# Kernel tuning notes

Measured on AMD Instinct MI355X. Metric: run time of the kernel, lower is better.

## Reference

```python
import jax, jax.numpy as jnp
import numpy as np

B, S, E = 2, 2048, 2048
H, KV, HD = 16, 4, 128          # attn heads, kv heads, head_dim = E//H
GROUPS = H // KV
I = 8192                        # intermediate_size
EPS = 1e-6
ROPE_THETA = 10000.0
SCALE = HD ** -0.5


def _rope_tables(seq_len, head_dim, dtype=jnp.float32):
    inv_freq = 1.0 / (ROPE_THETA ** (jnp.arange(0, head_dim, 2, dtype=jnp.float32) / head_dim))
    pos = jnp.arange(seq_len, dtype=jnp.float32)
    ang = pos[:, None] * inv_freq[None, :]            # [S, HD/2]
    emb = jnp.concatenate([ang, ang], axis=-1)        # [S, HD]
    return jnp.cos(emb).astype(dtype), jnp.sin(emb).astype(dtype)


def _rotate_half(x):
    x1, x2 = jnp.split(x, 2, axis=-1)
    return jnp.concatenate([-x2, x1], axis=-1)


def _apply_rope(x, cos, sin):
    # x: [B, h, S, HD]; cos/sin: [S, HD]
    return x * cos[None, None] + _rotate_half(x) * sin[None, None]


def _rmsnorm(x, w, eps=EPS):
    var = jnp.mean(jnp.square(x), axis=-1, keepdims=True)
    return x * jax.lax.rsqrt(var + eps) * w


def setup_inputs() -> dict:
    key = jax.random.key(0)
    ks = jax.random.split(key, 12)
    sd = lambda fan_in: 1.0 / np.sqrt(fan_in)
    inp = {
        "x": jax.random.normal(ks[0], (B, S, E), dtype=jnp.float32),
        "attn_mask": jnp.zeros((B, 1, S, S), dtype=jnp.bool_),
        "wq": jax.random.normal(ks[1], (E, E), dtype=jnp.float32) * sd(E),
        "bq": jnp.zeros((E,), dtype=jnp.float32),
        "wkv": jax.random.normal(ks[2], (2 * KV * HD, E), dtype=jnp.float32) * sd(E),
        "bkv": jnp.zeros((2 * KV * HD,), dtype=jnp.float32),
        "wo": jax.random.normal(ks[3], (E, E), dtype=jnp.float32) * sd(E),
        "w_gate": jax.random.normal(ks[4], (I, E), dtype=jnp.float32) * sd(E),
        "w_up": jax.random.normal(ks[5], (I, E), dtype=jnp.float32) * sd(E),
        "w_down": jax.random.normal(ks[6], (E, I), dtype=jnp.float32) * sd(I),
        "norm1_w": jnp.ones((E,), dtype=jnp.float32),
        "norm2_w": jnp.ones((E,), dtype=jnp.float32),
    }
    return inp


def reference(x, attn_mask, wq, bq, wkv, bkv, wo, w_gate, w_up, w_down, norm1_w, norm2_w):
    # ---- attention block ----
    y = _rmsnorm(x, norm1_w)
    q = y @ wq.T + bq                                     # [B,S,E]
    kv = y @ wkv.T + bkv                                  # [B,S,2*KV*HD]
    k, v = jnp.split(kv, 2, axis=-1)
    q = q.reshape(B, S, H, HD).transpose(0, 2, 1, 3)      # [B,H,S,HD]
    k = k.reshape(B, S, KV, HD).transpose(0, 2, 1, 3)     # [B,KV,S,HD]
    v = v.reshape(B, S, KV, HD).transpose(0, 2, 1, 3)
    cos, sin = _rope_tables(S, HD, dtype=q.dtype)
    q = _apply_rope(q, cos, sin)
    k = _apply_rope(k, cos, sin)
    # GQA expand kv heads
    k = jnp.repeat(k, GROUPS, axis=1)                     # [B,H,S,HD]
    v = jnp.repeat(v, GROUPS, axis=1)
    # NOTE: source Qwen2Attention.forward never applies attn_mask — faithful here.
    scores = jnp.einsum('bhsd,bhtd->bhst', q, k) * SCALE  # [B,H,S,S]
    attn = jax.nn.softmax(scores, axis=-1)
    o = jnp.einsum('bhst,bhtd->bhsd', attn, v)            # [B,H,S,HD]
    o = o.transpose(0, 2, 1, 3).reshape(B, S, E) @ wo.T
    x = x + o
    # ---- MLP block (SwiGLU) ----
    y = _rmsnorm(x, norm2_w)
    h = jax.nn.silu(y @ w_gate.T) * (y @ w_up.T)          # [B,S,I]
    x = x + h @ w_down.T
    return x
```

## Files before the change

kernel.cpp:

```cpp
#include <hip/hip_runtime.h>

typedef __bf16 bf16;
typedef __bf16 bf16x8 __attribute__((ext_vector_type(8)));
typedef __bf16 bf16x4 __attribute__((ext_vector_type(4)));
typedef float f32x4 __attribute__((ext_vector_type(4)));

#define DEV __device__ __forceinline__

constexpr int B_ = 2, S_ = 2048, E_ = 2048, H_ = 16, KVH_ = 4, HD_ = 128, I_ = 8192;
constexpr int KVROW = 2 * KVH_ * HD_;
constexpr float EPS_ = 1e-6f;
constexpr float SCALE_ = 0.08838834764831845f;

DEV void gload_lds16(const bf16* g, bf16* l) {
  __builtin_amdgcn_global_load_lds(
      (const __attribute__((address_space(1))) void*)g,
      (__attribute__((address_space(3))) void*)l, 16, 0, 0);
}

__global__ __launch_bounds__(256) void cvt_k(const float* __restrict__ src,
                                             bf16* __restrict__ dst, int n) {
  for (int i = (blockIdx.x * 256 + threadIdx.x) * 8; i < n; i += gridDim.x * 256 * 8) {
    const float4* p = (const float4*)(src + i);
    float4 a = p[0], b = p[1];
    bf16x8 o;
    o[0] = (bf16)a.x; o[1] = (bf16)a.y; o[2] = (bf16)a.z; o[3] = (bf16)a.w;
    o[4] = (bf16)b.x; o[5] = (bf16)b.y; o[6] = (bf16)b.z; o[7] = (bf16)b.w;
    *(bf16x8*)(dst + i) = o;
  }
}

template <typename InT>
__global__ __launch_bounds__(256) void rmsnorm_k(const InT* __restrict__ x,
                                                 const float* __restrict__ w,
                                                 bf16* __restrict__ y) {
  const int row = blockIdx.x, t = threadIdx.x;
  const size_t base = (size_t)row * E_ + t * 8;
  float v[8];
  if constexpr (sizeof(InT) == 2) {
    bf16x8 d = *(const bf16x8*)(x + base);
#pragma unroll
    for (int j = 0; j < 8; ++j) v[j] = (float)d[j];
  } else {
    const float4* p = (const float4*)(x + base);
    float4 a = p[0], b2 = p[1];
    v[0]=a.x; v[1]=a.y; v[2]=a.z; v[3]=a.w; v[4]=b2.x; v[5]=b2.y; v[6]=b2.z; v[7]=b2.w;
  }
  float ss = 0.f;
#pragma unroll
  for (int j = 0; j < 8; ++j) ss += v[j] * v[j];
#pragma unroll
  for (int off = 32; off; off >>= 1) ss += __shfl_xor(ss, off);
  __shared__ float red[4];
  if ((t & 63) == 0) red[t >> 6] = ss;
  __syncthreads();
  ss = red[0] + red[1] + red[2] + red[3];
  const float sc = rsqrtf(ss * (1.0f / E_) + EPS_);
  const float4* wp = (const float4*)(w + t * 8);
  float4 wa = wp[0], wb = wp[1];
  float wv[8] = {wa.x, wa.y, wa.z, wa.w, wb.x, wb.y, wb.z, wb.w};
  bf16x8 o;
#pragma unroll
  for (int j = 0; j < 8; ++j) o[j] = (bf16)(v[j] * sc * wv[j]);
  *(bf16x8*)(y + base) = o;
}

__global__ __launch_bounds__(256) void rope_k(bf16* __restrict__ q, bf16* __restrict__ kvb) {
  const int gid = blockIdx.x * 256 + threadIdx.x;
  const int d = gid & 63;
  const int r = gid >> 6;
  const int hh = r % (H_ + KVH_);
  const int s = (r / (H_ + KVH_)) % S_;
  const int b = r / ((H_ + KVH_) * S_);
  bf16* p = (hh < H_) ? (q + (size_t)(b * S_ + s) * E_ + hh * HD_)
                      : (kvb + (size_t)(b * S_ + s) * KVROW + (hh - H_) * HD_);
  const float invf = exp2f(-(float)d * (13.287712379549449f / 64.f));
  float sn, cs;
  sincosf((float)s * invf, &sn, &cs);
  const float x1 = (float)p[d], x2 = (float)p[d + 64];
  p[d] = (bf16)(x1 * cs - x2 * sn);
  p[d + 64] = (bf16)(x2 * cs + x1 * sn);
}

template <int EPI, bool WB>
__global__ __launch_bounds__(256, 2) void gemm_bt(const bf16* __restrict__ A,
                                                  const void* __restrict__ Wp,
                                                  const float* __restrict__ bias,
                                                  const void* __restrict__ ext,
                                                  void* __restrict__ out,
                                                  int M, int N, int K) {
  constexpr int BK = 64;
  __shared__ bf16 As[128 * BK];
  __shared__ bf16 Bs[128 * BK];
  const int t = threadIdx.x, lane = t & 63, w = t >> 6;
  const int g = lane >> 4, l15 = lane & 15;
  const int bm = blockIdx.y, bn = blockIdx.x;
  const int wm = w >> 1, wn = w & 1;
  f32x4 acc[4][4];
#pragma unroll
  for (int i = 0; i < 4; ++i)
#pragma unroll
    for (int j = 0; j < 4; ++j) acc[i][j] = {0.f, 0.f, 0.f, 0.f};

  const bf16* Ab = A + (size_t)bm * 128 * K;

  for (int k0 = 0; k0 < K; k0 += BK) {
    __syncthreads();
#pragma unroll
    for (int i = 0; i < 4; ++i) {
      const int c = t + i * 256;
      const int row = c >> 3, slot = c & 7;
      gload_lds16(Ab + (size_t)row * K + k0 + ((slot ^ (row & 7)) << 3), &As[c * 8]);
    }
    if constexpr (WB) {
      const bf16* Wb = (const bf16*)Wp + (size_t)bn * 128 * K;
#pragma unroll
      for (int i = 0; i < 4; ++i) {
        const int c = t + i * 256;
        const int row = c >> 3, slot = c & 7;
        gload_lds16(Wb + (size_t)row * K + k0 + ((slot ^ (row & 7)) << 3), &Bs[c * 8]);
      }
    } else {
      const float* Wb = (const float*)Wp + (size_t)bn * 128 * K;
#pragma unroll
      for (int i = 0; i < 4; ++i) {
        const int c = t + i * 256;
        const int row = c >> 3, slot = c & 7;
        const float4* wp = (const float4*)(Wb + (size_t)row * K + k0 + slot * 8);
        float4 w0 = wp[0], w1 = wp[1];
        bf16x8 pk;
        pk[0] = (bf16)w0.x; pk[1] = (bf16)w0.y; pk[2] = (bf16)w0.z; pk[3] = (bf16)w0.w;
        pk[4] = (bf16)w1.x; pk[5] = (bf16)w1.y; pk[6] = (bf16)w1.z; pk[7] = (bf16)w1.w;
        *(bf16x8*)&Bs[row * BK + ((slot ^ (row & 7)) << 3)] = pk;
      }
    }
    __syncthreads();
#pragma unroll
    for (int ks = 0; ks < 2; ++ks) {
      bf16x8 af[4], bfv[4];
#pragma unroll
      for (int mt = 0; mt < 4; ++mt) {
        const int row = wm * 64 + mt * 16 + l15;
        af[mt] = *(const bf16x8*)&As[row * BK + (((ks * 4 + g) ^ (row & 7)) << 3)];
      }
#pragma unroll
      for (int nt = 0; nt < 4; ++nt) {
        const int row = wn * 64 + nt * 16 + l15;
        bfv[nt] = *(const bf16x8*)&Bs[row * BK + (((ks * 4 + g) ^ (row & 7)) << 3)];
      }
#pragma unroll
      for (int mt = 0; mt < 4; ++mt)
#pragma unroll
        for (int nt = 0; nt < 4; ++nt)
          acc[mt][nt] = __builtin_amdgcn_mfma_f32_16x16x32_bf16(af[mt], bfv[nt], acc[mt][nt], 0, 0, 0);
    }
  }

  const int row0 = bm * 128 + wm * 64;
  const int col0 = bn * 128 + wn * 64;
#pragma unroll
  for (int nt = 0; nt < 4; ++nt) {
    const int col = col0 + nt * 16 + l15;
    const float bv = bias ? bias[col] : 0.f;
#pragma unroll
    for (int mt = 0; mt < 4; ++mt) {
#pragma unroll
      for (int r = 0; r < 4; ++r) {
        const int rowi = row0 + mt * 16 + g * 4 + r;
        const size_t idx = (size_t)rowi * N + col;
        float v = acc[mt][nt][r] + bv;
        if constexpr (EPI == 0) {
          ((bf16*)out)[idx] = (bf16)v;
        } else if constexpr (EPI == 1) {
          v += ((const float*)ext)[idx];
          ((bf16*)out)[idx] = (bf16)v;
        } else if constexpr (EPI == 2) {
          const float gv = (float)((const bf16*)ext)[idx];
          const float sg = gv / (1.f + __expf(-gv));
          ((bf16*)out)[idx] = (bf16)(sg * v);
        } else {
          v += (float)((const bf16*)ext)[idx];
          ((float*)out)[idx] = v;
        }
      }
    }
  }
}

__global__ __launch_bounds__(256, 2) void attn_k(const bf16* __restrict__ qb,
                                                 const bf16* __restrict__ kvb,
                                                 bf16* __restrict__ ob) {
  __shared__ bf16 Ks[64 * 128];
  __shared__ bf16 Vt[128 * 64];
  __shared__ bf16 Ps[4][32 * 64];
  const int t = threadIdx.x, lane = t & 63, w = t >> 6;
  const int g = lane >> 4, l15 = lane & 15;
  const int b = blockIdx.z, h = blockIdx.y;
  const int kvh = h >> 2;
  const int q0 = blockIdx.x * 128 + w * 32;

  bf16x8 qf[2][4];
#pragma unroll
  for (int qt = 0; qt < 2; ++qt)
#pragma unroll
    for (int ks = 0; ks < 4; ++ks)
      qf[qt][ks] = *(const bf16x8*)(qb + (size_t)(b * S_ + q0 + qt * 16 + l15) * E_ + h * HD_ + ks * 32 + g * 8);

  f32x4 o[8][2];
#pragma unroll
  for (int i = 0; i < 8; ++i) { o[i][0] = {0.f,0.f,0.f,0.f}; o[i][1] = {0.f,0.f,0.f,0.f}; }
  float mA[2] = {-1e30f, -1e30f}, lA[2] = {0.f, 0.f};

  for (int s0 = 0; s0 < S_; s0 += 64) {
    __syncthreads();
#pragma unroll
    for (int i = 0; i < 4; ++i) {
      const int c = t + i * 256;
      const int row = c >> 4, slot = c & 15;
      gload_lds16(kvb + (size_t)(b * S_ + s0 + row) * KVROW + kvh * HD_ + ((slot ^ (row & 15)) << 3),
                  &Ks[c * 8]);
    }
#pragma unroll
    for (int i = 0; i < 4; ++i) {
      const int c = t + i * 256;
      const int d = c & 127, kvc = c >> 7;
      const bf16* vs = kvb + (size_t)(b * S_ + s0 + kvc * 8) * KVROW + KVH_ * HD_ + kvh * HD_ + d;
      bf16x8 pk;
#pragma unroll
      for (int j = 0; j < 8; ++j) pk[j] = vs[(size_t)j * KVROW];
      *(bf16x8*)&Vt[d * 64 + ((kvc ^ (d & 7)) << 3)] = pk;
    }
    __syncthreads();

    f32x4 sc[2][4];
#pragma unroll
    for (int qt = 0; qt < 2; ++qt)
#pragma unroll
      for (int c = 0; c < 4; ++c) sc[qt][c] = {0.f,0.f,0.f,0.f};
#pragma unroll
    for (int ks = 0; ks < 4; ++ks) {
      bf16x8 kf[4];
#pragma unroll
      for (int c = 0; c < 4; ++c) {
        const int kv = c * 16 + l15;
        kf[c] = *(const bf16x8*)&Ks[kv * 128 + (((ks * 4 + g) ^ (kv & 15)) << 3)];
      }
#pragma unroll
      for (int c = 0; c < 4; ++c) {
        sc[0][c] = __builtin_amdgcn_mfma_f32_16x16x32_bf16(kf[c], qf[0][ks], sc[0][c], 0, 0, 0);
        sc[1][c] = __builtin_amdgcn_mfma_f32_16x16x32_bf16(kf[c], qf[1][ks], sc[1][c], 0, 0, 0);
      }
    }

    float corr[2];
#pragma unroll
    for (int qt = 0; qt < 2; ++qt) {
      float tm = sc[qt][0][0];
#pragma unroll
      for (int c = 0; c < 4; ++c)
#pragma unroll
        for (int r = 0; r < 4; ++r) tm = fmaxf(tm, sc[qt][c][r]);
      tm = fmaxf(tm, __shfl_xor(tm, 16));
      tm = fmaxf(tm, __shfl_xor(tm, 32));
      const float mn = fmaxf(mA[qt], tm);
      corr[qt] = __expf((mA[qt] - mn) * SCALE_);
      mA[qt] = mn;
      float ps = 0.f;
      const int q = qt * 16 + l15;
#pragma unroll
      for (int c = 0; c < 4; ++c)
#pragma unroll
        for (int r = 0; r < 4; ++r) {
          const float p = __expf((sc[qt][c][r] - mn) * SCALE_);
          ps += p;
          const int kv = c * 16 + g * 4 + r;
          Ps[w][q * 64 + (((kv >> 3) ^ (q & 7)) << 3) + (kv & 7)] = (bf16)p;
        }
      ps += __shfl_xor(ps, 16);
      ps += __shfl_xor(ps, 32);
      lA[qt] = lA[qt] * corr[qt] + ps;
#pragma unroll
      for (int dt = 0; dt < 8; ++dt) o[dt][qt] *= corr[qt];
    }
    asm volatile("s_waitcnt lgkmcnt(0)" ::: "memory");
#pragma unroll
    for (int ks = 0; ks < 2; ++ks) {
      bf16x8 pf[2];
#pragma unroll
      for (int qt = 0; qt < 2; ++qt) {
        const int q = qt * 16 + l15;
        pf[qt] = *(const bf16x8*)&Ps[w][q * 64 + (((ks * 4 + g) ^ (q & 7)) << 3)];
      }
#pragma unroll
      for (int dt = 0; dt < 8; ++dt) {
        const int d = dt * 16 + l15;
        const bf16x8 vf = *(const bf16x8*)&Vt[d * 64 + (((ks * 4 + g) ^ (d & 7)) << 3)];
        o[dt][0] = __builtin_amdgcn_mfma_f32_16x16x32_bf16(vf, pf[0], o[dt][0], 0, 0, 0);
        o[dt][1] = __builtin_amdgcn_mfma_f32_16x16x32_bf16(vf, pf[1], o[dt][1], 0, 0, 0);
      }
    }
  }

  const float inv0 = 1.f / lA[0], inv1 = 1.f / lA[1];
  __syncthreads();
  bf16* bb = (w < 2) ? &Ks[(w & 1) * 4096] : &Vt[(w & 1) * 4096];
#pragma unroll
  for (int dt = 0; dt < 8; ++dt)
#pragma unroll
    for (int qt = 0; qt < 2; ++qt) {
      const float iv = qt ? inv1 : inv0;
      bf16x4 pk;
#pragma unroll
      for (int r = 0; r < 4; ++r) pk[r] = (bf16)(o[dt][qt][r] * iv);
      const int q = qt * 16 + l15;
      const int s16 = (dt * 2 + (g >> 1)) ^ (q & 15);
      *(bf16x4*)&bb[q * 128 + (s16 << 3) + ((g & 1) << 2)] = pk;
    }
  asm volatile("s_waitcnt lgkmcnt(0)" ::: "memory");
#pragma unroll
  for (int it = 0; it < 8; ++it) {
    const int c = lane + it * 64;
    const int q = c >> 4, s16 = c & 15;
    const bf16x8 vv = *(const bf16x8*)&bb[q * 128 + ((s16 ^ (q & 15)) << 3)];
    *(bf16x8*)(ob + (size_t)(b * S_ + q0 + q) * E_ + h * HD_ + s16 * 8) = vv;
  }
}

extern "C" void kernel_launch(void* const* d_in, const int* in_sizes, int n_in,
                              void* d_out, int out_size, void* d_ws, size_t ws_size,
                              hipStream_t stream) {
  const float* x   = (const float*)d_in[0];
  const float* wq  = (const float*)d_in[2];
  const float* bq  = (const float*)d_in[3];
  const float* wkv = (const float*)d_in[4];
  const float* bkv = (const float*)d_in[5];
  const float* wo  = (const float*)d_in[6];
  const float* wg  = (const float*)d_in[7];
  const float* wu  = (const float*)d_in[8];
  const float* wd  = (const float*)d_in[9];
  const float* n1  = (const float*)d_in[10];
  const float* n2  = (const float*)d_in[11];
  float* out = (float*)d_out;
  char* ws = (char*)d_ws;
  bf16* y  = (bf16*)(ws);
  bf16* q  = (bf16*)(ws + (16ull << 20));
  bf16* kv = (bf16*)(ws + (32ull << 20));
  bf16* x1 = (bf16*)(ws + (40ull << 20));
  bf16* gh = (bf16*)(ws + (56ull << 20));
  bf16* o  = y;
  bf16* y2 = y;
  bf16* wqb  = (bf16*)(ws + (120ull << 20));
  bf16* wkvb = (bf16*)(ws + (128ull << 20));
  bf16* wob  = (bf16*)(ws + (132ull << 20));
  bf16* wgb  = (bf16*)(ws + (140ull << 20));
  bf16* wub  = (bf16*)(ws + (172ull << 20));
  bf16* wdb  = (bf16*)(ws + (204ull << 20));
  const int M = B_ * S_;
  const bool tierA = ws_size >= (236ull << 20);

  if (tierA) {
    cvt_k<<<512, 256, 0, stream>>>(wq,  wqb,  E_ * E_);
    cvt_k<<<512, 256, 0, stream>>>(wkv, wkvb, KVROW * E_);
    cvt_k<<<512, 256, 0, stream>>>(wo,  wob,  E_ * E_);
    cvt_k<<<512, 256, 0, stream>>>(wg,  wgb,  I_ * E_);
    cvt_k<<<512, 256, 0, stream>>>(wu,  wub,  I_ * E_);
    cvt_k<<<512, 256, 0, stream>>>(wd,  wdb,  E_ * I_);
  }

  rmsnorm_k<float><<<M, 256, 0, stream>>>(x, n1, y);
  if (tierA) {
    gemm_bt<0, true><<<dim3(E_ / 128, M / 128), 256, 0, stream>>>(y, wqb, bq, nullptr, q, M, E_, E_);
    gemm_bt<0, true><<<dim3(KVROW / 128, M / 128), 256, 0, stream>>>(y, wkvb, bkv, nullptr, kv, M, KVROW, E_);
  } else {
    gemm_bt<0, false><<<dim3(E_ / 128, M / 128), 256, 0, stream>>>(y, wq, bq, nullptr, q, M, E_, E_);
    gemm_bt<0, false><<<dim3(KVROW / 128, M / 128), 256, 0, stream>>>(y, wkv, bkv, nullptr, kv, M, KVROW, E_);
  }
  rope_k<<<(B_ * S_ * (H_ + KVH_) * 64) / 256, 256, 0, stream>>>(q, kv);
  attn_k<<<dim3(S_ / 128, H_, B_), 256, 0, stream>>>(q, kv, o);
  if (tierA) {
    gemm_bt<1, true><<<dim3(E_ / 128, M / 128), 256, 0, stream>>>(o, wob, nullptr, x, x1, M, E_, E_);
    rmsnorm_k<bf16><<<M, 256, 0, stream>>>(x1, n2, y2);
    gemm_bt<0, true><<<dim3(I_ / 128, M / 128), 256, 0, stream>>>(y2, wgb, nullptr, nullptr, gh, M, I_, E_);
    gemm_bt<2, true><<<dim3(I_ / 128, M / 128), 256, 0, stream>>>(y2, wub, nullptr, gh, gh, M, I_, E_);
    gemm_bt<3, true><<<dim3(E_ / 128, M / 128), 256, 0, stream>>>(gh, wdb, nullptr, x1, out, M, E_, I_);
  } else {
    gemm_bt<1, false><<<dim3(E_ / 128, M / 128), 256, 0, stream>>>(o, wo, nullptr, x, x1, M, E_, E_);
    rmsnorm_k<bf16><<<M, 256, 0, stream>>>(x1, n2, y2);
    gemm_bt<0, false><<<dim3(I_ / 128, M / 128), 256, 0, stream>>>(y2, wg, nullptr, nullptr, gh, M, I_, E_);
    gemm_bt<2, false><<<dim3(I_ / 128, M / 128), 256, 0, stream>>>(y2, wu, nullptr, gh, gh, M, I_, E_);
    gemm_bt<3, false><<<dim3(E_ / 128, M / 128), 256, 0, stream>>>(gh, wd, nullptr, x1, out, M, E_, I_);
  }
}
```

Measured before the change: 805.4 us.

## Fuse gate/up GEMMs with SwiGLU epilogue and merge weight conversions

Replaces the separate gate and up projection GEMMs with a single kernel that shares the activation tile, accumulates both outputs and applies SiLU*up in the epilogue. This avoids writing and re-reading the gate intermediate and loading the activations twice. The six per-weight fp32-to-bf16 conversion launches are also merged into one kernel over the contiguous destination buffer. Doubling the accumulators raises register pressure, which may lower occupancy or cause spills.

```diff
diff --git a/kernel.cpp b/kernel.cpp
--- a/kernel.cpp
+++ b/kernel.cpp
@@ -18,14 +18,27 @@
       (__attribute__((address_space(3))) void*)l, 16, 0, 0);
 }
 
-__global__ __launch_bounds__(256) void cvt_k(const float* __restrict__ src,
-                                             bf16* __restrict__ dst, int n) {
-  for (int i = (blockIdx.x * 256 + threadIdx.x) * 8; i < n; i += gridDim.x * 256 * 8) {
-    const float4* p = (const float4*)(src + i);
+__global__ __launch_bounds__(256) void cvt6_k(const float* __restrict__ s0, const float* __restrict__ s1,
+                                              const float* __restrict__ s2, const float* __restrict__ s3,
+                                              const float* __restrict__ s4, const float* __restrict__ s5,
+                                              bf16* __restrict__ dst) {
+  constexpr size_t N0 = 4194304, N1 = 2097152, N2 = 4194304,
+                   N3 = 16777216, N4 = 16777216, N5 = 16777216;
+  constexpr size_t TOT = N0 + N1 + N2 + N3 + N4 + N5;
+  for (size_t i = ((size_t)blockIdx.x * 256 + threadIdx.x) * 8; i < TOT;
+       i += (size_t)gridDim.x * 256 * 8) {
+    size_t off = i; const float* sp;
+    if (off < N0) sp = s0;
+    else if ((off -= N0) < N1) sp = s1;
+    else if ((off -= N1) < N2) sp = s2;
+    else if ((off -= N2) < N3) sp = s3;
+    else if ((off -= N3) < N4) sp = s4;
+    else { off -= N4; sp = s5; }
+    const float4* p = (const float4*)(sp + off);
     float4 a = p[0], b = p[1];
     bf16x8 o;
-    o[0] = (bf16)a.x; o[1] = (bf16)a.y; o[2] = (bf16)a.z; o[3] = (bf16)a.w;
-    o[4] = (bf16)b.x; o[5] = (bf16)b.y; o[6] = (bf16)b.z; o[7] = (bf16)b.w;
+    o[0]=(bf16)a.x; o[1]=(bf16)a.y; o[2]=(bf16)a.z; o[3]=(bf16)a.w;
+    o[4]=(bf16)b.x; o[5]=(bf16)b.y; o[6]=(bf16)b.z; o[7]=(bf16)b.w;
     *(bf16x8*)(dst + i) = o;
   }
 }
@@ -80,6 +93,84 @@
   const float x1 = (float)p[d], x2 = (float)p[d + 64];
   p[d] = (bf16)(x1 * cs - x2 * sn);
   p[d + 64] = (bf16)(x2 * cs + x1 * sn);
+}
+
+__global__ __launch_bounds__(256, 2) void gemm_gu(const bf16* __restrict__ A,
+                                                  const bf16* __restrict__ Wg,
+                                                  const bf16* __restrict__ Wu,
+                                                  bf16* __restrict__ out,
+                                                  int M, int N, int K) {
+  constexpr int BK = 64;
+  __shared__ bf16 As[128 * BK];
+  __shared__ bf16 Bg[128 * BK];
+  __shared__ bf16 Bu[128 * BK];
+  const int t = threadIdx.x, lane = t & 63, w = t >> 6;
+  const int g = lane >> 4, l15 = lane & 15;
+  const int bm = blockIdx.y, bn = blockIdx.x;
+  const int wm = w >> 1, wn = w & 1;
+  f32x4 ag[4][4], au[4][4];
+#pragma unroll
+  for (int i = 0; i < 4; ++i)
+#pragma unroll
+    for (int j = 0; j < 4; ++j) { ag[i][j] = {0.f,0.f,0.f,0.f}; au[i][j] = {0.f,0.f,0.f,0.f}; }
+
+  const bf16* Ab  = A  + (size_t)bm * 128 * K;
+  const bf16* Wgb = Wg + (size_t)bn * 128 * K;
+  const bf16* Wub = Wu + (size_t)bn * 128 * K;
+
+  for (int k0 = 0; k0 < K; k0 += BK) {
+    __syncthreads();
+#pragma unroll
+    for (int i = 0; i < 4; ++i) {
+      const int c = t + i * 256;
+      const int row = c >> 3, slot = c & 7;
+      const size_t goff = (size_t)row * K + k0 + ((slot ^ (row & 7)) << 3);
+      gload_lds16(Ab + goff, &As[c * 8]);
+      gload_lds16(Wgb + goff, &Bg[c * 8]);
+      gload_lds16(Wub + goff, &Bu[c * 8]);
+    }
+    __syncthreads();
+#pragma unroll
+    for (int ks = 0; ks < 2; ++ks) {
+      bf16x8 af[4], bgv[4], buv[4];
+#pragma unroll
+      for (int mt = 0; mt < 4; ++mt) {
+        const int row = wm * 64 + mt * 16 + l15;
+        af[mt] = *(const bf16x8*)&As[row * BK + (((ks * 4 + g) ^ (row & 7)) << 3)];
+      }
+#pragma unroll
+      for (int nt = 0; nt < 4; ++nt) {
+        const int row = wn * 64 + nt * 16 + l15;
+        const int off = row * BK + (((ks * 4 + g) ^ (row & 7)) << 3);
+        bgv[nt] = *(const bf16x8*)&Bg[off];
+        buv[nt] = *(const bf16x8*)&Bu[off];
+      }
+#pragma unroll
+      for (int mt = 0; mt < 4; ++mt)
+#pragma unroll
+        for (int nt = 0; nt < 4; ++nt) {
+          ag[mt][nt] = __builtin_amdgcn_mfma_f32_16x16x32_bf16(af[mt], bgv[nt], ag[mt][nt], 0, 0, 0);
+          au[mt][nt] = __builtin_amdgcn_mfma_f32_16x16x32_bf16(af[mt], buv[nt], au[mt][nt], 0, 0, 0);
+        }
+    }
+  }
+
+  const int row0 = bm * 128 + wm * 64;
+  const int col0 = bn * 128 + wn * 64;
+#pragma unroll
+  for (int nt = 0; nt < 4; ++nt) {
+    const int col = col0 + nt * 16 + l15;
+#pragma unroll
+    for (int mt = 0; mt < 4; ++mt) {
+#pragma unroll
+      for (int r = 0; r < 4; ++r) {
+        const int rowi = row0 + mt * 16 + g * 4 + r;
+        const float gv = ag[mt][nt][r];
+        const float hv = (gv / (1.f + __expf(-gv))) * au[mt][nt][r];
+        out[(size_t)rowi * N + col] = (bf16)hv;
+      }
+    }
+  }
 }
 
 template <int EPI, bool WB>
@@ -358,14 +449,8 @@
   const int M = B_ * S_;
   const bool tierA = ws_size >= (236ull << 20);
 
-  if (tierA) {
-    cvt_k<<<512, 256, 0, stream>>>(wq,  wqb,  E_ * E_);
-    cvt_k<<<512, 256, 0, stream>>>(wkv, wkvb, KVROW * E_);
-    cvt_k<<<512, 256, 0, stream>>>(wo,  wob,  E_ * E_);
-    cvt_k<<<512, 256, 0, stream>>>(wg,  wgb,  I_ * E_);
-    cvt_k<<<512, 256, 0, stream>>>(wu,  wub,  I_ * E_);
-    cvt_k<<<512, 256, 0, stream>>>(wd,  wdb,  E_ * I_);
-  }
+  if (tierA)
+    cvt6_k<<<2048, 256, 0, stream>>>(wq, wkv, wo, wg, wu, wd, wqb);
 
   rmsnorm_k<float><<<M, 256, 0, stream>>>(x, n1, y);
   if (tierA) {
@@ -380,8 +465,7 @@
   if (tierA) {
     gemm_bt<1, true><<<dim3(E_ / 128, M / 128), 256, 0, stream>>>(o, wob, nullptr, x, x1, M, E_, E_);
     rmsnorm_k<bf16><<<M, 256, 0, stream>>>(x1, n2, y2);
-    gemm_bt<0, true><<<dim3(I_ / 128, M / 128), 256, 0, stream>>>(y2, wgb, nullptr, nullptr, gh, M, I_, E_);
-    gemm_bt<2, true><<<dim3(I_ / 128, M / 128), 256, 0, stream>>>(y2, wub, nullptr, gh, gh, M, I_, E_);
+    gemm_gu<<<dim3(I_ / 128, M / 128), 256, 0, stream>>>(y2, wgb, wub, gh, M, I_, E_);
     gemm_bt<3, true><<<dim3(E_ / 128, M / 128), 256, 0, stream>>>(gh, wdb, nullptr, x1, out, M, E_, I_);
   } else {
     gemm_bt<1, false><<<dim3(E_ / 128, M / 128), 256, 0, stream>>>(o, wo, nullptr, x, x1, M, E_, E_);
```

New measurement: 754.9 us. -6.3%, faster.
